# Performance work log

Measured on AMD Instinct MI355X. Metric: run time of the kernel, lower is better.

Reference implementation:

```python
import jax, jax.numpy as jnp
from jax import lax
import numpy as np

WS = 8      # window_size
SS = 4      # shift_size
NH = 8      # num_heads
DIM = 192
HID = int(DIM * 2.66)  # 510


def _rel_pos_index(ws):
    coords = np.stack(np.meshgrid(np.arange(ws), np.arange(ws), indexing='ij'))
    flat = coords.reshape(2, -1)
    rel = (flat[:, :, None] - flat[:, None, :]).transpose(1, 2, 0)
    rel[..., 0] += ws - 1
    rel[..., 1] += ws - 1
    rel[..., 0] *= 2 * ws - 1
    return rel.sum(-1)  # (ws*ws, ws*ws) int


def _attn_mask(Hp, Wp, ws, ss):
    img = np.zeros((Hp, Wp), dtype=np.float32)
    slices = (slice(0, -ws), slice(-ws, -ss), slice(-ss, None))
    cnt = 0
    for h in slices:
        for w in slices:
            img[h, w] = cnt
            cnt += 1
    mw = img.reshape(Hp // ws, ws, Wp // ws, ws).transpose(0, 2, 1, 3).reshape(-1, ws * ws)
    am = mw[:, None, :] - mw[:, :, None]
    return np.where(am != 0, -100.0, 0.0).astype(np.float32)  # (nW, N, N)


def _ln(t, w, b):
    mu = t.mean(-1, keepdims=True)
    var = t.var(-1, keepdims=True)
    return (t - mu) / jnp.sqrt(var + 1e-5) * w + b


def setup_inputs() -> dict:
    key = jax.random.key(0)
    ks = jax.random.split(key, 12)
    s = 0.05
    return {
        'x': jax.random.normal(ks[0], (2, DIM, 256, 256), jnp.float32),
        'norm1_w': jnp.ones((DIM,), jnp.float32),
        'norm1_b': jnp.zeros((DIM,), jnp.float32),
        'qkv_w': jax.random.normal(ks[1], (3 * DIM, DIM), jnp.float32) * s,
        'rpb_table': jax.random.normal(ks[2], ((2 * WS - 1) * (2 * WS - 1), NH), jnp.float32) * 0.02,
        'proj_w': jax.random.normal(ks[3], (DIM, DIM), jnp.float32) * s,
        'proj_b': jnp.zeros((DIM,), jnp.float32),
        'norm2_w': jnp.ones((DIM,), jnp.float32),
        'norm2_b': jnp.zeros((DIM,), jnp.float32),
        'pin_w': jax.random.normal(ks[4], (2 * HID, DIM), jnp.float32) * s,
        'dw_w': jax.random.normal(ks[5], (2 * HID, 1, 3, 3), jnp.float32) * s,
        'pout_w': jax.random.normal(ks[6], (DIM, HID), jnp.float32) * s,
    }


def reference(x, norm1_w, norm1_b, qkv_w, rpb_table, proj_w, proj_b,
              norm2_w, norm2_b, pin_w, dw_w, pout_w):
    B, C, H, W = x.shape
    hd = C // NH
    scale = hd ** -0.5

    # ---- norm1 (channel-last layernorm) ----
    xc = jnp.transpose(x, (0, 2, 3, 1))  # BHWC
    xn = _ln(xc, norm1_w, norm1_b)

    # ---- pad to window multiple ----
    pad_b = (WS - H % WS) % WS
    pad_r = (WS - W % WS) % WS
    xn = jnp.pad(xn, ((0, 0), (0, pad_b), (0, pad_r), (0, 0)))
    Hp, Wp = H + pad_b, W + pad_r

    # ---- cyclic shift ----
    sx = jnp.roll(xn, (-SS, -SS), axis=(1, 2))

    # ---- window partition ----
    nH, nW = Hp // WS, Wp // WS
    N = WS * WS
    xw = sx.reshape(B, nH, WS, nW, WS, C).transpose(0, 1, 3, 2, 4, 5)
    xw = xw.reshape(B * nH * nW, N, C)

    # ---- window attention ----
    qkv = (xw @ qkv_w.T).reshape(-1, N, 3, NH, hd).transpose(2, 0, 3, 1, 4)
    q, k, v = qkv[0] * scale, qkv[1], qkv[2]  # (B_, NH, N, hd)
    attn = jnp.einsum('bhnd,bhmd->bhnm', q, k)

    idx = _rel_pos_index(WS)
    bias = rpb_table[idx.reshape(-1)].reshape(N, N, NH).transpose(2, 0, 1)
    attn = attn + bias[None]

    mask = jnp.asarray(_attn_mask(Hp, Wp, WS, SS))  # (nWtot, N, N)
    nWtot = nH * nW
    attn = attn.reshape(B, nWtot, NH, N, N) + mask[None, :, None]
    attn = jax.nn.softmax(attn.reshape(-1, NH, N, N), axis=-1)

    out = jnp.einsum('bhnm,bhmd->bhnd', attn, v)
    out = out.transpose(0, 2, 1, 3).reshape(-1, N, C)
    out = out @ proj_w.T + proj_b

    # ---- window reverse + unshift + crop ----
    out = out.reshape(B, nH, nW, WS, WS, C).transpose(0, 1, 3, 2, 4, 5)
    out = out.reshape(B, Hp, Wp, C)
    out = jnp.roll(out, (SS, SS), axis=(1, 2))[:, :H, :W]
    x = x + jnp.transpose(out, (0, 3, 1, 2))

    # ---- FFN: 1x1 in -> depthwise 3x3 -> gated gelu -> 1x1 out ----
    y = _ln(jnp.transpose(x, (0, 2, 3, 1)), norm2_w, norm2_b)
    y = jnp.transpose(y, (0, 3, 1, 2))
    y = jnp.einsum('bchw,oc->bohw', y, pin_w)
    y = lax.conv_general_dilated(y, dw_w, (1, 1), 'SAME',
                                 feature_group_count=dw_w.shape[0],
                                 dimension_numbers=('NCHW', 'OIHW', 'NCHW'))
    h = dw_w.shape[0] // 2
    y = jax.nn.gelu(y[:, :h], approximate=False) * y[:, h:]
    y = jnp.einsum('bchw,oc->bohw', y, pout_w)
    return x + y
```

## Files before the change

kernel.cpp:

```cpp
#include <hip/hip_runtime.h>
#include <hip/hip_bf16.h>
#include <math.h>

#define CDIM 192
#define NTOK 131072
#define HD 24
#define NHEADS 8
#define NTC 65536

typedef __attribute__((ext_vector_type(4))) float floatx4;
typedef __attribute__((ext_vector_type(8))) short bf16x8;

static __device__ __forceinline__ float bf2f(__hip_bfloat16 h) { return __bfloat162float(h); }
static __device__ __forceinline__ __hip_bfloat16 f2bf(float f) { return __float2bfloat16(f); }
static __device__ __forceinline__ float s2f(short s) {
  union { unsigned u; float f; } c; c.u = ((unsigned)(unsigned short)s) << 16; return c.f;
}
static __device__ __forceinline__ short f2s(float f) {
  __hip_bfloat16 h = __float2bfloat16(f);
  union { __hip_bfloat16 h; short s; } c; c.h = h; return c.s;
}
static __device__ __forceinline__ void load_lds16(const void* g, void* l) {
  __builtin_amdgcn_global_load_lds(
      (const __attribute__((address_space(1))) void*)g,
      (__attribute__((address_space(3))) void*)l, 16, 0, 0);
}

__global__ __launch_bounds__(256) void kcvt(
    const float* __restrict__ in, __hip_bfloat16* __restrict__ out, int n) {
  int i = blockIdx.x * 256 + threadIdx.x;
  if (i < n) out[i] = f2bf(in[i]);
}

__global__ __launch_bounds__(256) void k0_padpout(
    const float* __restrict__ w, __hip_bfloat16* __restrict__ o) {
  int idx = blockIdx.x * 256 + threadIdx.x;
  int n = idx >> 9, k = idx & 511;
  o[idx] = (k < 510) ? f2bf(w[n * 510 + k]) : f2bf(0.f);
}

__global__ __launch_bounds__(256) void k0_padpin(
    const float* __restrict__ w, const float* __restrict__ nw,
    __hip_bfloat16* __restrict__ o) {
  int idx = blockIdx.x * 256 + threadIdx.x;
  int n = idx / 192, k = idx % 192;
  int src = (n < 510) ? n : ((n >= 512 && n < 1022) ? n - 2 : -1);
  o[idx] = (src >= 0) ? f2bf(w[src * 192 + k] * nw[k]) : f2bf(0.f);
}

__global__ __launch_bounds__(256) void k0_st(
    const float* __restrict__ w, const float* __restrict__ nw,
    const float* __restrict__ nb, float* __restrict__ S, float* __restrict__ T) {
  int n = blockIdx.x * 256 + threadIdx.x;
  int src = (n < 510) ? n : ((n >= 512 && n < 1022) ? n - 2 : -1);
  float s = 0.f, t = 0.f;
  if (src >= 0)
    for (int c = 0; c < 192; ++c) {
      float v = w[src * 192 + c];
      s += v * nw[c]; t += v * nb[c];
    }
  S[n] = s; T[n] = t;
}

__global__ __launch_bounds__(256) void k0_wtap(
    const float* __restrict__ wdw, __hip_bfloat16* __restrict__ wa,
    __hip_bfloat16* __restrict__ wg) {
  int idx = blockIdx.x * 256 + threadIdx.x;
  if (idx >= 9 * 512) return;
  int tap = idx >> 9, c = idx & 511;
  wa[idx] = (c < 510) ? f2bf(wdw[c * 9 + tap]) : f2bf(0.f);
  wg[idx] = (c < 510) ? f2bf(wdw[(c + 510) * 9 + tap]) : f2bf(0.f);
}

__global__ __launch_bounds__(256) void k1_ln_raster(
    const float* __restrict__ x,
    const float* __restrict__ w,
    const float* __restrict__ bsh,
    __hip_bfloat16* __restrict__ out) {
  __shared__ float xs[32][193];
  int bid = blockIdx.x;
  int b = bid >> 11, si = (bid >> 3) & 255, sj0 = (bid & 7) << 5;
  int i = (si + 4) & 255;
  int tid = threadIdx.x;
  int lane = tid & 63, wv = tid >> 6;
  int p0 = (lane & 7) << 2;
  int cb = wv * 8 + (lane >> 3);
  int j4 = (sj0 + p0 + 4) & 255;
  long pbase = ((long)(b * CDIM + cb) << 16) + (i << 8) + j4;
  #pragma unroll
  for (int co = 0; co < 6; ++co) {
    floatx4 v = *(const floatx4*)(x + pbase + ((long)co << 21));
    int c = co * 32 + cb;
    xs[p0 + 0][c] = v[0];
    xs[p0 + 1][c] = v[1];
    xs[p0 + 2][c] = v[2];
    xs[p0 + 3][c] = v[3];
  }
  __syncthreads();
  int c0 = lane * 3;
  float w0 = w[c0], w1 = w[c0 + 1], w2 = w[c0 + 2];
  float g0 = bsh[c0], g1 = bsh[c0 + 1], g2 = bsh[c0 + 2];
  long tok0 = ((long)b << 16) + (si << 8) + sj0;
  for (int it = 0; it < 8; ++it) {
    int p = (wv << 3) + it;
    float v0 = xs[p][c0], v1 = xs[p][c0 + 1], v2 = xs[p][c0 + 2];
    float s = v0 + v1 + v2;
    float sq = v0 * v0 + v1 * v1 + v2 * v2;
    for (int off = 32; off; off >>= 1) { s += __shfl_xor(s, off); sq += __shfl_xor(sq, off); }
    float mean = s * (1.0f / 192.0f);
    float var  = sq * (1.0f / 192.0f) - mean * mean;
    float rstd = rsqrtf(var + 1e-5f);
    short* rowp = (short*)&xs[p][0];
    rowp[c0    ] = f2s((v0 - mean) * rstd * w0 + g0);
    rowp[c0 + 1] = f2s((v1 - mean) * rstd * w1 + g1);
    rowp[c0 + 2] = f2s((v2 - mean) * rstd * w2 + g2);
  }
  __syncthreads();
  char* gout = (char*)out + tok0 * 384;
  #pragma unroll
  for (int k = 0; k < 3; ++k) {
    int o = k * 4096 + tid * 16;
    int pt = o / 384, iw = (o % 384) >> 2;
    floatx4 v = {xs[pt][iw], xs[pt][iw + 1], xs[pt][iw + 2], xs[pt][iw + 3]};
    *(floatx4*)(gout + o) = v;
  }
}

template <int WM, int WN, int EPI>
__global__ __launch_bounds__(256) void gemm_lds(
    const __hip_bfloat16* __restrict__ A,
    const __hip_bfloat16* __restrict__ B,
    const float* __restrict__ bias,
    __hip_bfloat16* __restrict__ C,
    int K, int lda, int ldb, int ldc) {
  constexpr int BM = 32 * WM, BN = 32 * WN;
  __shared__ __hip_bfloat16 As[BM * 32];
  __shared__ __hip_bfloat16 Bs[BN * 32];
  int t = threadIdx.x;
  int wave = t >> 6, lane = t & 63;
  int wm = wave >> 1, wn = wave & 1;
  int r16 = lane & 15, quad = lane >> 4;
  long m0 = (long)blockIdx.y * BM;
  long n0 = (long)blockIdx.x * BN;
  int srow = t >> 2, scol = (t & 3) << 3;
  floatx4 acc[WM][WN];
  for (int i = 0; i < WM; ++i)
    for (int j = 0; j < WN; ++j)
      acc[i][j] = (floatx4){0.f, 0.f, 0.f, 0.f};
  for (int k0 = 0; k0 < K; k0 += 32) {
    __syncthreads();
    for (int p = 0; p < WM / 2; ++p)
      load_lds16(A + (m0 + srow + p * 64) * lda + k0 + scol,
                 (char*)As + t * 16 + p * 4096);
    for (int p = 0; p < WN / 2; ++p)
      load_lds16(B + (n0 + srow + p * 64) * ldb + k0 + scol,
                 (char*)Bs + t * 16 + p * 4096);
    __syncthreads();
    bf16x8 af[WM], bf[WN];
    for (int i = 0; i < WM; ++i)
      af[i] = *(const bf16x8*)&As[(wm * 16 * WM + i * 16 + r16) * 32 + quad * 8];
    for (int j = 0; j < WN; ++j)
      bf[j] = *(const bf16x8*)&Bs[(wn * 16 * WN + j * 16 + r16) * 32 + quad * 8];
    for (int i = 0; i < WM; ++i)
      for (int j = 0; j < WN; ++j)
        acc[i][j] = __builtin_amdgcn_mfma_f32_16x16x32_bf16(af[i], bf[j], acc[i][j], 0, 0, 0);
  }
  for (int i = 0; i < WM; ++i)
    for (int j = 0; j < WN; ++j) {
      int col = n0 + wn * 16 * WN + j * 16 + r16;
      float badd = (EPI == 1) ? bias[col] : 0.f;
      for (int r = 0; r < 4; ++r) {
        long row = m0 + wm * 16 * WM + i * 16 + quad * 4 + r;
        C[row * ldc + col] = f2bf(acc[i][j][r] + badd);
      }
    }
}

__global__ __launch_bounds__(256) void gemm_qkv(
    const __hip_bfloat16* __restrict__ A,
    const __hip_bfloat16* __restrict__ B,
    __hip_bfloat16* __restrict__ C) {
  constexpr int WM = 4, WN = 2, BM = 128, BN = 64;
  __shared__ __hip_bfloat16 As[BM * 32];
  __shared__ __hip_bfloat16 Bs[BN * 32];
  int t = threadIdx.x;
  int wave = t >> 6, lane = t & 63;
  int wm = wave >> 1, wn = wave & 1;
  int r16 = lane & 15, quad = lane >> 4;
  long m0 = (long)blockIdx.y * BM;
  int n0 = blockIdx.x * BN;
  int srow = t >> 2, scol = (t & 3) << 3;
  floatx4 acc[WM][WN];
  for (int i = 0; i < WM; ++i)
    for (int j = 0; j < WN; ++j)
      acc[i][j] = (floatx4){0.f, 0.f, 0.f, 0.f};
  for (int k0 = 0; k0 < 192; k0 += 32) {
    __syncthreads();
    for (int p = 0; p < 2; ++p)
      load_lds16(A + (m0 + srow + p * 64) * 192 + k0 + scol,
                 (char*)As + t * 16 + p * 4096);
    load_lds16(B + (n0 + srow) * 192 + k0 + scol, (char*)Bs + t * 16);
    __syncthreads();
    bf16x8 af[WM], bf[WN];
    for (int i = 0; i < WM; ++i)
      af[i] = *(const bf16x8*)&As[(wm * 64 + i * 16 + r16) * 32 + quad * 8];
    for (int j = 0; j < WN; ++j)
      bf[j] = *(const bf16x8*)&Bs[(wn * 32 + j * 16 + r16) * 32 + quad * 8];
    for (int i = 0; i < WM; ++i)
      for (int j = 0; j < WN; ++j)
        acc[i][j] = __builtin_amdgcn_mfma_f32_16x16x32_bf16(af[i], bf[j], acc[i][j], 0, 0, 0);
  }
  for (int i = 0; i < WM; ++i)
    for (int j = 0; j < WN; ++j) {
      int col = n0 + wn * 32 + j * 16 + r16;
      int sel = col / 192;
      int cm = col - sel * 192;
      int h = (cm * 683) >> 14;
      int d = cm - h * 24;
      long cb = (long)sel * (NTC * 192) + (long)h * (NTC * 24) + d;
      for (int r = 0; r < 4; ++r) {
        long row = m0 + wm * 64 + i * 16 + quad * 4 + r;
        C[cb + row * 24] = f2bf(acc[i][j][r]);
      }
    }
}

__global__ __launch_bounds__(256) void gemm_pin(
    const __hip_bfloat16* __restrict__ x2,
    const __hip_bfloat16* __restrict__ B,
    const float* __restrict__ stats,
    const float* __restrict__ Sv,
    const float* __restrict__ Tv,
    __hip_bfloat16* __restrict__ C,
    int bb, int r0) {
  constexpr int WM = 4, WN = 4, BM = 128, BN = 128;
  __shared__ __hip_bfloat16 As[BM * 32];
  __shared__ __hip_bfloat16 Bs[BN * 32];
  int t = threadIdx.x;
  int wave = t >> 6, lane = t & 63;
  int wm = wave >> 1, wn = wave & 1;
  int r16 = lane & 15, quad = lane >> 4;
  int m0 = blockIdx.y * BM;
  int n0 = blockIdx.x * BN;
  int srow = t >> 2, scol = (t & 3) << 3;
  floatx4 acc[WM][WN];
  for (int i = 0; i < WM; ++i)
    for (int j = 0; j < WN; ++j)
      acc[i][j] = (floatx4){0.f, 0.f, 0.f, 0.f};
  for (int k0 = 0; k0 < 192; k0 += 32) {
    __syncthreads();
    for (int p = 0; p < 2; ++p) {
      int rr = m0 + srow + p * 64;
      int il = rr >> 8, jj = rr & 255;
      int gi = r0 - 1 + il; gi = gi < 0 ? 0 : (gi > 255 ? 255 : gi);
      long tok = ((long)bb << 16) + (gi << 8) + jj;
      load_lds16(x2 + tok * 192 + k0 + scol, (char*)As + t * 16 + p * 4096);
    }
    for (int p = 0; p < 2; ++p)
      load_lds16(B + (n0 + srow + p * 64) * 192 + k0 + scol,
                 (char*)Bs + t * 16 + p * 4096);
    __syncthreads();
    bf16x8 af[WM], bf[WN];
    for (int i = 0; i < WM; ++i)
      af[i] = *(const bf16x8*)&As[(wm * 64 + i * 16 + r16) * 32 + quad * 8];
    for (int j = 0; j < WN; ++j)
      bf[j] = *(const bf16x8*)&Bs[(wn * 64 + j * 16 + r16) * 32 + quad * 8];
    for (int i = 0; i < WM; ++i)
      for (int j = 0; j < WN; ++j)
        acc[i][j] = __builtin_amdgcn_mfma_f32_16x16x32_bf16(af[i], bf[j], acc[i][j], 0, 0, 0);
  }
  for (int i = 0; i < WM; ++i) {
    float mr[4], rsd[4];
    #pragma unroll
    for (int r = 0; r < 4; ++r) {
      int row = m0 + wm * 64 + i * 16 + quad * 4 + r;
      int il = row >> 8, jj = row & 255;
      int gi = r0 - 1 + il; gi = gi < 0 ? 0 : (gi > 255 ? 255 : gi);
      long tok = ((long)bb << 16) + (gi << 8) + jj;
      mr[r] = stats[2 * tok]; rsd[r] = stats[2 * tok + 1];
    }
    for (int j = 0; j < WN; ++j) {
      int col = n0 + wn * 64 + j * 16 + r16;
      float sv = Sv[col], tv = Tv[col];
      for (int r = 0; r < 4; ++r) {
        int row = m0 + wm * 64 + i * 16 + quad * 4 + r;
        C[(long)row * 1024 + col] = f2bf(acc[i][j][r] * rsd[r] - mr[r] * rsd[r] * sv + tv);
      }
    }
  }
}

__global__ __launch_bounds__(256) void gemm_pout(
    const __hip_bfloat16* __restrict__ A,
    const __hip_bfloat16* __restrict__ B,
    const __hip_bfloat16* __restrict__ x2,
    float* __restrict__ out,
    int b, int r0) {
  constexpr int WM = 2, WN = 4, BM = 64, BN = 128;
  __shared__ __hip_bfloat16 As[BM * 32];
  __shared__ __hip_bfloat16 Bs[BN * 32];
  int t = threadIdx.x;
  int wave = t >> 6, lane = t & 63;
  int wm = wave >> 1, wn = wave & 1;
  int r16 = lane & 15, quad = lane >> 4;
  long m0 = (long)blockIdx.y * BM;
  long n0 = (long)blockIdx.x * BN;
  int srow = t >> 2, scol = (t & 3) << 3;
  floatx4 acc[WM][WN];
  for (int i = 0; i < WM; ++i)
    for (int j = 0; j < WN; ++j)
      acc[i][j] = (floatx4){0.f, 0.f, 0.f, 0.f};
  for (int k0 = 0; k0 < 512; k0 += 32) {
    __syncthreads();
    load_lds16(A + (m0 + srow) * 512 + k0 + scol, (char*)As + t * 16);
    for (int p = 0; p < WN / 2; ++p)
      load_lds16(B + (n0 + srow + p * 64) * 512 + k0 + scol,
                 (char*)Bs + t * 16 + p * 4096);
    __syncthreads();
    bf16x8 af[WM], bf[WN];
    for (int i = 0; i < WM; ++i)
      af[i] = *(const bf16x8*)&As[(wm * 16 * WM + i * 16 + r16) * 32 + quad * 8];
    for (int j = 0; j < WN; ++j)
      bf[j] = *(const bf16x8*)&Bs[(wn * 16 * WN + j * 16 + r16) * 32 + quad * 8];
    for (int i = 0; i < WM; ++i)
      for (int j = 0; j < WN; ++j)
        acc[i][j] = __builtin_amdgcn_mfma_f32_16x16x32_bf16(af[i], bf[j], acc[i][j], 0, 0, 0);
  }
  for (int i = 0; i < WM; ++i)
    for (int j = 0; j < WN; ++j) {
      int p_ = n0 + wn * 16 * WN + j * 16 + r16;
      int il = p_ >> 8, jj = p_ & 255;
      long pix = ((long)(r0 + il) << 8) + jj;
      for (int r = 0; r < 4; ++r) {
        int c_ = m0 + wm * 16 * WM + i * 16 + quad * 4 + r;
        long tok = ((long)b << 16) + pix;
        float v = acc[i][j][r] + bf2f(x2[tok * CDIM + c_]);
        out[((long)(b * CDIM + c_) << 16) + pix] = v;
      }
    }
}

__global__ __launch_bounds__(256) void k3_attn(
    const __hip_bfloat16* __restrict__ qkv,
    const float* __restrict__ rpb,
    __hip_bfloat16* __restrict__ out,
    int wid0) {
  __shared__ alignas(16) short Kp[64 * 32];
  __shared__ alignas(16) short Vt[32 * 64];
  __shared__ alignas(16) short Ps[4][16 * 64];
  __shared__ float rpbs[225];
  int h = blockIdx.x, widl = blockIdx.y;
  int wid = wid0 + widl;
  int t = threadIdx.x;
  int wv = t >> 6, lane = t & 63, quad = lane >> 4, r16 = lane & 15;
  int wi_l = widl >> 5, wjl = widl & 31;
  const short* qk = (const short*)qkv;
  const short* Qp  = qk + (long)h * (NTC * 24);
  const short* Kpg = Qp + (long)NTC * 192;
  const short* Vpg = Qp + (long)NTC * 384;

  if (t < 225) rpbs[t] = rpb[t * NHEADS + h];

  {
    int kr = t >> 2, kq = t & 3;
    bf16x8 kv = {0, 0, 0, 0, 0, 0, 0, 0};
    if (kq < 3) {
      int ltok = ((((wi_l << 3) + (kr >> 3)) << 8) + (wjl << 3) + (kr & 7));
      kv = *(const bf16x8*)(Kpg + (long)ltok * 24 + kq * 8);
    }
    *(bf16x8*)&Kp[kr * 32 + ((kq ^ ((kr >> 1) & 3)) << 3)] = kv;
  }
  {
    int tok = t & 63, q8 = t >> 6;
    if (q8 < 3) {
      int ltok = ((((wi_l << 3) + (tok >> 3)) << 8) + (wjl << 3) + (tok & 7));
      bf16x8 vv = *(const bf16x8*)(Vpg + (long)ltok * 24 + q8 * 8);
      #pragma unroll
      for (int e = 0; e < 8; ++e) {
        int d = q8 * 8 + e;
        Vt[d * 64 + (((tok >> 3) ^ (d & 7)) << 3) + (tok & 7)] = vv[e];
      }
    } else {
      int zt = t - 192;
      int d = 24 + (zt >> 3), tokg = zt & 7;
      bf16x8 z = {0, 0, 0, 0, 0, 0, 0, 0};
      *(bf16x8*)&Vt[d * 64 + ((tokg ^ (d & 7)) << 3)] = z;
    }
  }
  bf16x8 qf;
  {
    int nn = wv * 16 + r16;
    int ltok = ((((wi_l << 3) + (nn >> 3)) << 8) + (wjl << 3) + (nn & 7));
    qf = *(const bf16x8*)(Qp + (long)ltok * 24 + quad * 8);
  }
  __syncthreads();

  floatx4 sj[4];
  int kswz = (quad ^ ((r16 >> 1) & 3)) << 3;
  #pragma unroll
  for (int j = 0; j < 4; ++j) {
    bf16x8 kf = *(const bf16x8*)&Kp[(j * 16 + r16) * 32 + kswz];
    sj[j] = __builtin_amdgcn_mfma_f32_16x16x32_bf16(
        qf, kf, (floatx4){0.f, 0.f, 0.f, 0.f}, 0, 0, 0);
  }

  int b = wid >> 10, wi = (wid >> 5) & 31, wj = wid & 31;
  int rkj[4];
  #pragma unroll
  for (int j = 0; j < 4; ++j) {
    int m = j * 16 + r16;
    int gsi = wi * 8 + (m >> 3), gsj = wj * 8 + (m & 7);
    rkj[j] = ((gsi < 248) ? 0 : (gsi < 252 ? 1 : 2)) * 3 +
             ((gsj < 248) ? 0 : (gsj < 252 ? 1 : 2));
  }

  float rs[4];
  #pragma unroll
  for (int r = 0; r < 4; ++r) {
    int n = wv * 16 + quad * 4 + r;
    int ti = n >> 3, tj = n & 7;
    int gi = wi * 8 + ti, gj = wj * 8 + tj;
    int rq = ((gi < 248) ? 0 : (gi < 252 ? 1 : 2)) * 3 +
             ((gj < 248) ? 0 : (gj < 252 ? 1 : 2));
    float val[4];
    float mx = -1e30f;
    #pragma unroll
    for (int j = 0; j < 4; ++j) {
      int m = j * 16 + r16;
      int idx = (ti - (m >> 3) + 7) * 15 + (tj - (m & 7) + 7);
      float v = sj[j][r] * 0.20412414523193154f + rpbs[idx];
      if (rkj[j] != rq) v -= 100.0f;
      val[j] = v;
      mx = fmaxf(mx, v);
    }
    #pragma unroll
    for (int off = 1; off < 16; off <<= 1) mx = fmaxf(mx, __shfl_xor(mx, off));
    float sum = 0.f;
    int row = quad * 4 + r;
    #pragma unroll
    for (int j = 0; j < 4; ++j) {
      float p = __expf(val[j] - mx);
      sum += p;
      int col = j * 16 + r16;
      Ps[wv][row * 64 + ((((col >> 3) ^ (row & 7)) << 3)) + (col & 7)] = f2s(p);
    }
    #pragma unroll
    for (int off = 1; off < 16; off <<= 1) sum += __shfl_xor(sum, off);
    rs[r] = 1.0f / sum;
  }
  __syncthreads();

  floatx4 o0 = {0.f, 0.f, 0.f, 0.f}, o1 = {0.f, 0.f, 0.f, 0.f};
  #pragma unroll
  for (int kk = 0; kk < 2; ++kk) {
    int g = (((kk * 4 + quad) ^ (r16 & 7)) << 3);
    bf16x8 pa = *(const bf16x8*)&Ps[wv][r16 * 64 + g];
    bf16x8 b0 = *(const bf16x8*)&Vt[r16 * 64 + g];
    bf16x8 b1 = *(const bf16x8*)&Vt[(16 + r16) * 64 + g];
    o0 = __builtin_amdgcn_mfma_f32_16x16x32_bf16(pa, b0, o0, 0, 0, 0);
    o1 = __builtin_amdgcn_mfma_f32_16x16x32_bf16(pa, b1, o1, 0, 0, 0);
  }
  #pragma unroll
  for (int r = 0; r < 4; ++r) {
    int n = wv * 16 + quad * 4 + r;
    int gi = wi * 8 + (n >> 3), gj = wj * 8 + (n & 7);
    long ob = (((long)b << 16) + (gi << 8) + gj) * CDIM + h * HD;
    out[ob + r16] = f2bf(o0[r] * rs[r]);
    if (r16 < 8) out[ob + 16 + r16] = f2bf(o1[r] * rs[r]);
  }
}

__global__ __launch_bounds__(256) void k4_res_raster(
    const float* __restrict__ x,
    const __hip_bfloat16* __restrict__ tmp,
    __hip_bfloat16* __restrict__ x2,
    float* __restrict__ stats) {
  __shared__ float xs[32][193];
  int bid = blockIdx.x;
  int b = bid >> 11, i = (bid >> 3) & 255, j0 = (bid & 7) << 5;
  int tid = threadIdx.x;
  int lane = tid & 63, wv = tid >> 6;
  int p0 = (lane & 7) << 2;
  int cb = wv * 8 + (lane >> 3);
  long pbase = ((long)(b * CDIM + cb) << 16) + (i << 8) + j0 + p0;
  #pragma unroll
  for (int co = 0; co < 6; ++co) {
    floatx4 v = *(const floatx4*)(x + pbase + ((long)co << 21));
    int c = co * 32 + cb;
    xs[p0 + 0][c] = v[0];
    xs[p0 + 1][c] = v[1];
    xs[p0 + 2][c] = v[2];
    xs[p0 + 3][c] = v[3];
  }
  __syncthreads();
  int c0 = lane * 3;
  int si = (i + 252) & 255;
  for (int it = 0; it < 8; ++it) {
    int p = (wv << 3) + it;
    int j = j0 + p;
    int sj = (j + 252) & 255;
    long tsh = ((long)b << 16) + (si << 8) + sj;
    long sb = tsh * CDIM + c0;
    float v0 = xs[p][c0    ] + bf2f(tmp[sb    ]);
    float v1 = xs[p][c0 + 1] + bf2f(tmp[sb + 1]);
    float v2 = xs[p][c0 + 2] + bf2f(tmp[sb + 2]);
    float s = v0 + v1 + v2, sq = v0 * v0 + v1 * v1 + v2 * v2;
    for (int off = 32; off; off >>= 1) { s += __shfl_xor(s, off); sq += __shfl_xor(sq, off); }
    float mean = s * (1.0f / 192.0f);
    float var  = sq * (1.0f / 192.0f) - mean * mean;
    float rstd = rsqrtf(var + 1e-5f);
    short* rowp = (short*)&xs[p][0];
    rowp[c0    ] = f2s(v0);
    rowp[c0 + 1] = f2s(v1);
    rowp[c0 + 2] = f2s(v2);
    if (lane == 0) {
      long t2 = ((long)b << 16) + (i << 8) + j;
      stats[2 * t2] = mean; stats[2 * t2 + 1] = rstd;
    }
  }
  __syncthreads();
  long t20 = ((long)b << 16) + (i << 8) + j0;
  char* gout = (char*)x2 + t20 * 384;
  #pragma unroll
  for (int k = 0; k < 3; ++k) {
    int o = k * 4096 + tid * 16;
    int pt = o / 384, iw = (o % 384) >> 2;
    floatx4 v = {xs[pt][iw], xs[pt][iw + 1], xs[pt][iw + 2], xs[pt][iw + 3]};
    *(floatx4*)(gout + o) = v;
  }
}

__global__ __launch_bounds__(256) void k7_dwgate(
    const __hip_bfloat16* __restrict__ pin,
    const __hip_bfloat16* __restrict__ wa,
    const __hip_bfloat16* __restrict__ wg,
    __hip_bfloat16* __restrict__ out,
    int r0) {
  int t = threadIdx.x;
  int oct = t & 63, pl = t >> 6;
  int p = blockIdx.x * 4 + pl;
  int il = p >> 8, j = p & 255;
  int gi = r0 + il;
  int c0 = oct << 3;
  float a[8], g[8];
  for (int e = 0; e < 8; ++e) { a[e] = 0.f; g[e] = 0.f; }
  for (int di = -1; di <= 1; ++di) {
    int ii = gi + di; if (ii < 0 || ii > 255) continue;
    int br = il + di + 1;
    for (int dj = -1; dj <= 1; ++dj) {
      int jj = j + dj; if (jj < 0 || jj > 255) continue;
      long nbase = ((long)((br << 8) + jj)) << 10;
      int tap = (di + 1) * 3 + (dj + 1);
      bf16x8 va  = *(const bf16x8*)((const short*)pin + nbase + c0);
      bf16x8 vg  = *(const bf16x8*)((const short*)pin + nbase + 512 + c0);
      bf16x8 wa8 = *(const bf16x8*)((const short*)wa + tap * 512 + c0);
      bf16x8 wg8 = *(const bf16x8*)((const short*)wg + tap * 512 + c0);
      for (int e = 0; e < 8; ++e) {
        a[e] += s2f(wa8[e]) * s2f(va[e]);
        g[e] += s2f(wg8[e]) * s2f(vg[e]);
      }
    }
  }
  bf16x8 r;
  for (int e = 0; e < 8; ++e) {
    float ge = 0.5f * a[e] * (1.0f + erff(a[e] * 0.70710678118654752f));
    r[e] = f2s(ge * g[e]);
  }
  *(bf16x8*)((short*)out + (long)p * 512 + c0) = r;
}

extern "C" void kernel_launch(void* const* d_in, const int* in_sizes, int n_in,
                              void* d_out, int out_size, void* d_ws, size_t ws_size,
                              hipStream_t stream) {
  const float* x       = (const float*)d_in[0];
  const float* norm1_w = (const float*)d_in[1];
  const float* norm1_b = (const float*)d_in[2];
  const float* qkv_w   = (const float*)d_in[3];
  const float* rpb     = (const float*)d_in[4];
  const float* proj_w  = (const float*)d_in[5];
  const float* proj_b  = (const float*)d_in[6];
  const float* norm2_w = (const float*)d_in[7];
  const float* norm2_b = (const float*)d_in[8];
  const float* pin_w   = (const float*)d_in[9];
  const float* dw_w    = (const float*)d_in[10];
  const float* pout_w  = (const float*)d_in[11];

  char* ws = (char*)d_ws;
  __hip_bfloat16* wsLN1 = (__hip_bfloat16*)(ws);
  __hip_bfloat16* wsPRJ = (__hip_bfloat16*)(ws);
  __hip_bfloat16* wsPINC= (__hip_bfloat16*)(ws);
  __hip_bfloat16* wsATT = (__hip_bfloat16*)(ws + 50331648UL);
  __hip_bfloat16* wsX2  = (__hip_bfloat16*)(ws + 50331648UL);
  float*          wsST  = (float*)         (ws + 100663296UL);
  __hip_bfloat16* wsGT  = (__hip_bfloat16*)(ws + 101711872UL);
  __hip_bfloat16* wsWA  = (__hip_bfloat16*)(ws + 118489088UL);
  __hip_bfloat16* wsWG  = (__hip_bfloat16*)(ws + 118507520UL);
  float*          wsS   = (float*)         (ws + 118517760UL);
  float*          wsT   = (float*)         (ws + 118525952UL);
  __hip_bfloat16* wsPW  = (__hip_bfloat16*)(ws + 120586240UL);
  __hip_bfloat16* wsQW  = (__hip_bfloat16*)(ws + 120782848UL);
  __hip_bfloat16* wsPJW = (__hip_bfloat16*)(ws + 121004032UL);
  __hip_bfloat16* wsPIW = (__hip_bfloat16*)(ws + 121077760UL);
  float* out = (float*)d_out;
  __hip_bfloat16* qkvbuf = (__hip_bfloat16*)d_out;

  kcvt<<<(110592 + 255) / 256, 256, 0, stream>>>(qkv_w, wsQW, 110592);
  kcvt<<<(36864 + 255) / 256, 256, 0, stream>>>(proj_w, wsPJW, 36864);
  k0_padpout<<<384, 256, 0, stream>>>(pout_w, wsPW);
  k0_padpin<<<768, 256, 0, stream>>>(pin_w, norm2_w, wsPIW);
  k0_st<<<4, 256, 0, stream>>>(pin_w, norm2_w, norm2_b, wsS, wsT);
  k0_wtap<<<18, 256, 0, stream>>>(dw_w, wsWA, wsWG);
  k1_ln_raster<<<4096, 256, 0, stream>>>(x, norm1_w, norm1_b, wsLN1);
  for (int b = 0; b < 2; ++b) {
    gemm_qkv<<<dim3(9, 512), 256, 0, stream>>>(
        wsLN1 + (long)b * 65536 * CDIM, wsQW, qkvbuf);
    k3_attn<<<dim3(8, 1024), 256, 0, stream>>>(qkvbuf, rpb, wsATT, b * 1024);
  }
  gemm_lds<4, 2, 1><<<dim3(3, 1024), 256, 0, stream>>>(
      wsATT, wsPJW, proj_b, wsPRJ, 192, 192, 192, 192);
  k4_res_raster<<<4096, 256, 0, stream>>>(x, wsPRJ, wsX2, wsST);
  for (int cc = 0; cc < 8; ++cc) {
    int b = cc >> 2, r0 = (cc & 3) * 64;
    gemm_pin<<<dim3(8, 132), 256, 0, stream>>>(
        wsX2, wsPIW, wsST, wsS, wsT, wsPINC, b, r0);
    k7_dwgate<<<4096, 256, 0, stream>>>(wsPINC, wsWA, wsWG, wsGT, r0);
    gemm_pout<<<dim3(128, 3), 256, 0, stream>>>(wsPW, wsGT, wsX2, out, b, r0);
  }
}
```

Before: 925.3 us.

## Pad per-head QKV stride to 32 and restructure layernorm kernels to 8 threads per token

The QKV GEMM epilogue now writes each head's tokens with a 32-element stride instead of 24, so attention loads are aligned and use shift addressing, with Q fragments masked for the padded quad. Both layernorm kernels switch from one wave per token row to 8 threads per token with 24 channels each, doing an 8-lane shuffle reduction and writing packed bf16 directly to global memory. This removes the second LDS pass and barrier, and the residual kernel reads tmp with 16-byte vector loads. The padded QKV buffer needs about a third more memory, and the caller's allocation must have been enlarged to match, which is not visible here.

```diff
diff --git a/kernel.cpp b/kernel.cpp
--- a/kernel.cpp
+++ b/kernel.cpp
@@ -10,6 +10,7 @@
 
 typedef __attribute__((ext_vector_type(4))) float floatx4;
 typedef __attribute__((ext_vector_type(8))) short bf16x8;
+typedef __attribute__((ext_vector_type(4))) unsigned int uintx4;
 
 static __device__ __forceinline__ float bf2f(__hip_bfloat16 h) { return __bfloat162float(h); }
 static __device__ __forceinline__ __hip_bfloat16 f2bf(float f) { return __float2bfloat16(f); }
@@ -78,11 +79,13 @@
     const float* __restrict__ bsh,
     __hip_bfloat16* __restrict__ out) {
   __shared__ float xs[32][193];
+  __shared__ float wls[192], bls[192];
   int bid = blockIdx.x;
   int b = bid >> 11, si = (bid >> 3) & 255, sj0 = (bid & 7) << 5;
   int i = (si + 4) & 255;
   int tid = threadIdx.x;
   int lane = tid & 63, wv = tid >> 6;
+  if (tid < 192) { wls[tid] = w[tid]; bls[tid] = bsh[tid]; }
   int p0 = (lane & 7) << 2;
   int cb = wv * 8 + (lane >> 3);
   int j4 = (sj0 + p0 + 4) & 255;
@@ -97,33 +100,29 @@
     xs[p0 + 3][c] = v[3];
   }
   __syncthreads();
-  int c0 = lane * 3;
-  float w0 = w[c0], w1 = w[c0 + 1], w2 = w[c0 + 2];
-  float g0 = bsh[c0], g1 = bsh[c0 + 1], g2 = bsh[c0 + 2];
+  int p = tid >> 3, q = tid & 7, c0 = q * 24;
+  float v[24], s = 0.f, sq = 0.f;
+  #pragma unroll
+  for (int e = 0; e < 24; ++e) {
+    float t = xs[p][c0 + e]; v[e] = t; s += t; sq += t * t;
+  }
+  #pragma unroll
+  for (int off = 1; off < 8; off <<= 1) { s += __shfl_xor(s, off); sq += __shfl_xor(sq, off); }
+  float mean = s * (1.0f / 192.0f);
+  float var  = sq * (1.0f / 192.0f) - mean * mean;
+  float rstd = rsqrtf(var + 1e-5f);
+  unsigned pk[12];
+  #pragma unroll
+  for (int e = 0; e < 12; ++e) {
+    unsigned lo = (unsigned short)f2s((v[2*e  ] - mean) * rstd * wls[c0 + 2*e  ] + bls[c0 + 2*e  ]);
+    unsigned hi = (unsigned short)f2s((v[2*e+1] - mean) * rstd * wls[c0 + 2*e+1] + bls[c0 + 2*e+1]);
+    pk[e] = lo | (hi << 16);
+  }
   long tok0 = ((long)b << 16) + (si << 8) + sj0;
-  for (int it = 0; it < 8; ++it) {
-    int p = (wv << 3) + it;
-    float v0 = xs[p][c0], v1 = xs[p][c0 + 1], v2 = xs[p][c0 + 2];
-    float s = v0 + v1 + v2;
-    float sq = v0 * v0 + v1 * v1 + v2 * v2;
-    for (int off = 32; off; off >>= 1) { s += __shfl_xor(s, off); sq += __shfl_xor(sq, off); }
-    float mean = s * (1.0f / 192.0f);
-    float var  = sq * (1.0f / 192.0f) - mean * mean;
-    float rstd = rsqrtf(var + 1e-5f);
-    short* rowp = (short*)&xs[p][0];
-    rowp[c0    ] = f2s((v0 - mean) * rstd * w0 + g0);
-    rowp[c0 + 1] = f2s((v1 - mean) * rstd * w1 + g1);
-    rowp[c0 + 2] = f2s((v2 - mean) * rstd * w2 + g2);
-  }
-  __syncthreads();
-  char* gout = (char*)out + tok0 * 384;
-  #pragma unroll
-  for (int k = 0; k < 3; ++k) {
-    int o = k * 4096 + tid * 16;
-    int pt = o / 384, iw = (o % 384) >> 2;
-    floatx4 v = {xs[pt][iw], xs[pt][iw + 1], xs[pt][iw + 2], xs[pt][iw + 3]};
-    *(floatx4*)(gout + o) = v;
-  }
+  char* gout = (char*)out + (tok0 + p) * 384 + q * 48;
+  *(uintx4*)(gout     ) = (uintx4){pk[0], pk[1], pk[2], pk[3]};
+  *(uintx4*)(gout + 16) = (uintx4){pk[4], pk[5], pk[6], pk[7]};
+  *(uintx4*)(gout + 32) = (uintx4){pk[8], pk[9], pk[10], pk[11]};
 }
 
 template <int WM, int WN, int EPI>
@@ -217,10 +216,10 @@
       int cm = col - sel * 192;
       int h = (cm * 683) >> 14;
       int d = cm - h * 24;
-      long cb = (long)sel * (NTC * 192) + (long)h * (NTC * 24) + d;
+      long cb = (long)sel * (NTC * 256) + ((long)h << 21) + d;
       for (int r = 0; r < 4; ++r) {
         long row = m0 + wm * 64 + i * 16 + quad * 4 + r;
-        C[cb + row * 24] = f2bf(acc[i][j][r]);
+        C[cb + (row << 5)] = f2bf(acc[i][j][r]);
       }
     }
 }
@@ -355,9 +354,9 @@
   int wv = t >> 6, lane = t & 63, quad = lane >> 4, r16 = lane & 15;
   int wi_l = widl >> 5, wjl = widl & 31;
   const short* qk = (const short*)qkv;
-  const short* Qp  = qk + (long)h * (NTC * 24);
-  const short* Kpg = Qp + (long)NTC * 192;
-  const short* Vpg = Qp + (long)NTC * 384;
+  const short* Qp  = qk + ((long)h << 21);
+  const short* Kpg = Qp + (long)NTC * 256;
+  const short* Vpg = Qp + (long)NTC * 512;
 
   if (t < 225) rpbs[t] = rpb[t * NHEADS + h];
 
@@ -366,7 +365,7 @@
     bf16x8 kv = {0, 0, 0, 0, 0, 0, 0, 0};
     if (kq < 3) {
       int ltok = ((((wi_l << 3) + (kr >> 3)) << 8) + (wjl << 3) + (kr & 7));
-      kv = *(const bf16x8*)(Kpg + (long)ltok * 24 + kq * 8);
+      kv = *(const bf16x8*)(Kpg + ((long)ltok << 5) + kq * 8);
     }
     *(bf16x8*)&Kp[kr * 32 + ((kq ^ ((kr >> 1) & 3)) << 3)] = kv;
   }
@@ -374,7 +373,7 @@
     int tok = t & 63, q8 = t >> 6;
     if (q8 < 3) {
       int ltok = ((((wi_l << 3) + (tok >> 3)) << 8) + (wjl << 3) + (tok & 7));
-      bf16x8 vv = *(const bf16x8*)(Vpg + (long)ltok * 24 + q8 * 8);
+      bf16x8 vv = *(const bf16x8*)(Vpg + ((long)ltok << 5) + q8 * 8);
       #pragma unroll
       for (int e = 0; e < 8; ++e) {
         int d = q8 * 8 + e;
@@ -387,11 +386,11 @@
       *(bf16x8*)&Vt[d * 64 + ((tokg ^ (d & 7)) << 3)] = z;
     }
   }
-  bf16x8 qf;
-  {
+  bf16x8 qf = {0, 0, 0, 0, 0, 0, 0, 0};
+  if (quad < 3) {
     int nn = wv * 16 + r16;
     int ltok = ((((wi_l << 3) + (nn >> 3)) << 8) + (wjl << 3) + (nn & 7));
-    qf = *(const bf16x8*)(Qp + (long)ltok * 24 + quad * 8);
+    qf = *(const bf16x8*)(Qp + ((long)ltok << 5) + quad * 8);
   }
   __syncthreads();
 
@@ -493,41 +492,42 @@
     xs[p0 + 3][c] = v[3];
   }
   __syncthreads();
-  int c0 = lane * 3;
-  int si = (i + 252) & 255;
-  for (int it = 0; it < 8; ++it) {
-    int p = (wv << 3) + it;
-    int j = j0 + p;
-    int sj = (j + 252) & 255;
-    long tsh = ((long)b << 16) + (si << 8) + sj;
-    long sb = tsh * CDIM + c0;
-    float v0 = xs[p][c0    ] + bf2f(tmp[sb    ]);
-    float v1 = xs[p][c0 + 1] + bf2f(tmp[sb + 1]);
-    float v2 = xs[p][c0 + 2] + bf2f(tmp[sb + 2]);
-    float s = v0 + v1 + v2, sq = v0 * v0 + v1 * v1 + v2 * v2;
-    for (int off = 32; off; off >>= 1) { s += __shfl_xor(s, off); sq += __shfl_xor(sq, off); }
-    float mean = s * (1.0f / 192.0f);
-    float var  = sq * (1.0f / 192.0f) - mean * mean;
-    float rstd = rsqrtf(var + 1e-5f);
-    short* rowp = (short*)&xs[p][0];
-    rowp[c0    ] = f2s(v0);
-    rowp[c0 + 1] = f2s(v1);
-    rowp[c0 + 2] = f2s(v2);
-    if (lane == 0) {
-      long t2 = ((long)b << 16) + (i << 8) + j;
-      stats[2 * t2] = mean; stats[2 * t2 + 1] = rstd;
-    }
-  }
-  __syncthreads();
-  long t20 = ((long)b << 16) + (i << 8) + j0;
-  char* gout = (char*)x2 + t20 * 384;
-  #pragma unroll
-  for (int k = 0; k < 3; ++k) {
-    int o = k * 4096 + tid * 16;
-    int pt = o / 384, iw = (o % 384) >> 2;
-    floatx4 v = {xs[pt][iw], xs[pt][iw + 1], xs[pt][iw + 2], xs[pt][iw + 3]};
-    *(floatx4*)(gout + o) = v;
-  }
+  int p = tid >> 3, q = tid & 7, c0 = q * 24;
+  int j = j0 + p;
+  int si = (i + 252) & 255, sj = (j + 252) & 255;
+  long tsh = ((long)b << 16) + (si << 8) + sj;
+  const short* tp = (const short*)tmp + tsh * 192 + c0;
+  bf16x8 t0 = *(const bf16x8*)(tp);
+  bf16x8 t1 = *(const bf16x8*)(tp + 8);
+  bf16x8 t2v = *(const bf16x8*)(tp + 16);
+  float v[24], s = 0.f, sq = 0.f;
+  #pragma unroll
+  for (int e = 0; e < 8; ++e) {
+    float a0 = xs[p][c0 + e     ] + s2f(t0[e]);
+    float a1 = xs[p][c0 + e + 8 ] + s2f(t1[e]);
+    float a2 = xs[p][c0 + e + 16] + s2f(t2v[e]);
+    v[e] = a0; v[e + 8] = a1; v[e + 16] = a2;
+    s += a0 + a1 + a2;
+    sq += a0 * a0 + a1 * a1 + a2 * a2;
+  }
+  #pragma unroll
+  for (int off = 1; off < 8; off <<= 1) { s += __shfl_xor(s, off); sq += __shfl_xor(sq, off); }
+  float mean = s * (1.0f / 192.0f);
+  float var  = sq * (1.0f / 192.0f) - mean * mean;
+  float rstd = rsqrtf(var + 1e-5f);
+  long t2g = ((long)b << 16) + (i << 8) + j;
+  if (q == 0) { stats[2 * t2g] = mean; stats[2 * t2g + 1] = rstd; }
+  unsigned pk[12];
+  #pragma unroll
+  for (int e = 0; e < 12; ++e) {
+    unsigned lo = (unsigned short)f2s(v[2 * e]);
+    unsigned hi = (unsigned short)f2s(v[2 * e + 1]);
+    pk[e] = lo | (hi << 16);
+  }
+  char* gout = (char*)x2 + t2g * 384 + q * 48;
+  *(uintx4*)(gout     ) = (uintx4){pk[0], pk[1], pk[2], pk[3]};
+  *(uintx4*)(gout + 16) = (uintx4){pk[4], pk[5], pk[6], pk[7]};
+  *(uintx4*)(gout + 32) = (uintx4){pk[8], pk[9], pk[10], pk[11]};
 }
 
 __global__ __launch_bounds__(256) void k7_dwgate(
```

After: 929.7 us. No clear change (+0.5%).
